# Optimization experiments

Measured on AMD Instinct MI355X. Metric: run time of the kernel, lower is better.

The kernel has to match this reference:

```python
import jax, jax.numpy as jnp
import numpy as np

N = 65536
D_MODEL = 8
D_STATE = 16
D_INNER = 16  # d_model * expand
PK = 12       # sqrt(144)
NE = 144
EH = 16
GH = 4
NH = 4
PEER_IN = GH + 2 * D_MODEL + 2   # 22
GRU_IN = 2 + 2 * D_MODEL          # 18
RESCALE = 0.1


def setup_inputs() -> dict:
    key = jax.random.key(0)
    ks = iter(jax.random.split(key, 40))
    rn = lambda shape, s=0.02: jax.random.normal(next(ks), shape, dtype=jnp.float32) * s
    inp = {
        'grad': jax.random.normal(next(ks), (N,), dtype=jnp.float32),
        'sharpness': jax.random.uniform(next(ks), (N,), dtype=jnp.float32),
        'gru_state': jnp.zeros((N, GH), jnp.float32),
        'mfwd_state': jnp.zeros((D_INNER, D_STATE), jnp.float32),
        'mbwd_state': jnp.zeros((D_INNER, D_STATE), jnp.float32),
        # input_proj: Linear(2, d_model, bias=True)
        'inproj_W': rn((D_MODEL, 2), 0.5), 'inproj_b': jnp.zeros((D_MODEL,), jnp.float32),
        # two Mamba3ScanBlocks stacked on leading axis: [0]=fwd, [1]=bwd
        'm_inW': rn((2, 2 * D_INNER, D_MODEL), 0.2),
        'm_dtW': rn((2, D_INNER, D_INNER), 0.2), 'm_dtb': jnp.zeros((2, D_INNER), jnp.float32),
        'm_BW': rn((2, D_STATE, D_INNER), 0.2), 'm_CW': rn((2, D_STATE, D_INNER), 0.2),
        'm_Alog': jnp.broadcast_to(jnp.log(jnp.linspace(1.0, D_STATE, D_STATE, dtype=jnp.float32))[None, None, :], (2, D_INNER, D_STATE)).copy(),
        'm_D': jnp.ones((2, D_INNER), jnp.float32),
        'm_rope': rn((2, D_INNER, D_STATE), 0.01),
        'm_outW': rn((2, D_MODEL, D_INNER), 0.2),
        # MiniGRU: Linear(22, 4) x3
        'gru_Wz': rn((GH, GRU_IN + GH), 0.2), 'gru_bz': jnp.zeros((GH,), jnp.float32),
        'gru_Wr': rn((GH, GRU_IN + GH), 0.2), 'gru_br': jnp.zeros((GH,), jnp.float32),
        'gru_Wh': rn((GH, GRU_IN + GH), 0.2), 'gru_bh': jnp.zeros((GH,), jnp.float32),
        # PEER heads (stacked over heads)
        'peer_qW': rn((NH, D_MODEL, PEER_IN), 0.2),
        'keysA': rn((NH, PK, D_MODEL // 2), 0.02),
        'keysB': rn((NH, PK, D_MODEL // 2), 0.02),
        # shared expert pool
        'eW1': rn((NE, EH, 1), 0.02), 'eb1': jnp.zeros((NE, EH), jnp.float32),
        'eW2': rn((NE, 1, EH), 0.02), 'eb2': jnp.zeros((NE, 1), jnp.float32),
    }
    return inp


def _mamba_scan(x, h0, inW, dtW, dtb, BW, CW, Alog, Dp, rope, outW):
    # x: [N, d_model]; h0: [d_inner, d_state]
    xz = x @ inW.T                       # [N, 2*d_inner]
    xb, z = xz[:, :D_INNER], xz[:, D_INNER:]
    dt = jax.nn.softplus(xb @ dtW.T + dtb)   # [N, d_inner]
    B = xb @ BW.T                            # [N, d_state]
    C = xb @ CW.T                            # [N, d_state]
    A = -jnp.exp(Alog)                       # [d_inner, d_state]

    def step(h, t):
        dt_i, B_i, C_i, xb_i = t
        dti = dt_i[:, None]                                # [d_inner, 1]
        A_bar = (1.0 + dti * A * 0.5) / (1.0 - dti * A * 0.5 + 1e-8)
        ph = dti * rope
        h_rot = h * jnp.cos(ph) - jnp.roll(h, 1, axis=-1) * jnp.sin(ph)
        h_new = A_bar * h_rot + (dti * B_i[None, :]) * xb_i[:, None]
        y = (h_new * C_i[None, :]).sum(-1)                 # [d_inner]
        return h_new, y

    h_final, ys = jax.lax.scan(step, h0, (dt, B, C, xb))
    y = ys * jax.nn.silu(z) + Dp[None, :] * xb
    return y @ outW.T, h_final


def reference(grad, sharpness, gru_state, mfwd_state, mbwd_state,
              inproj_W, inproj_b,
              m_inW, m_dtW, m_dtb, m_BW, m_CW, m_Alog, m_D, m_rope, m_outW,
              gru_Wz, gru_bz, gru_Wr, gru_br, gru_Wh, gru_bh,
              peer_qW, keysA, keysB, eW1, eb1, eW2, eb2):
    g = grad.reshape(-1).astype(jnp.float32)
    s = sharpness.reshape(-1).astype(jnp.float32)
    sort_idx = jnp.argsort(jnp.abs(g))
    gs, ss = g[sort_idx], s[sort_idx]

    x = jnp.stack([gs, ss], axis=-1) @ inproj_W.T + inproj_b   # [N, d_model]

    fwd_out, new_fwd = _mamba_scan(x, mfwd_state, m_inW[0], m_dtW[0], m_dtb[0],
                                   m_BW[0], m_CW[0], m_Alog[0], m_D[0], m_rope[0], m_outW[0])
    bwd_out, new_bwd = _mamba_scan(x[::-1], mbwd_state, m_inW[1], m_dtW[1], m_dtb[1],
                                   m_BW[1], m_CW[1], m_Alog[1], m_D[1], m_rope[1], m_outW[1])
    bwd_out = bwd_out[::-1]

    unsort = jnp.argsort(sort_idx)
    fwd_ctx = fwd_out[unsort]
    bwd_ctx = bwd_out[unsort]

    # MiniGRU
    gru_in = jnp.concatenate([g[:, None], s[:, None], fwd_ctx, bwd_ctx], axis=-1)  # [N, 18]
    h = gru_state.astype(jnp.float32)
    xh = jnp.concatenate([gru_in, h], axis=-1)
    zg = jax.nn.sigmoid(xh @ gru_Wz.T + gru_bz)
    r = jax.nn.sigmoid(xh @ gru_Wr.T + gru_br)
    xrh = jnp.concatenate([gru_in, r * h], axis=-1)
    h_t = jnp.tanh(xrh @ gru_Wh.T + gru_bh)
    new_gru = (1.0 - zg) * h + zg * h_t

    # PEER routing (4 heads, product keys)
    peer_in = jnp.concatenate([new_gru, fwd_ctx, bwd_ctx, g[:, None], s[:, None]], axis=-1)  # [N, 22]
    half = D_MODEL // 2
    total = jnp.zeros((g.shape[0], 1), jnp.float32)
    for hidx in range(NH):
        q = peer_in @ peer_qW[hidx].T                              # [N, d_model]
        idx_a = jnp.argmax(q[:, :half] @ keysA[hidx].T, axis=-1)   # [N]
        idx_b = jnp.argmax(q[:, half:] @ keysB[hidx].T, axis=-1)
        eidx = idx_a * PK + idx_b                                  # [N]
        z1 = jax.nn.relu(eW1[eidx][:, :, 0] * g[:, None] + eb1[eidx])   # [N, EH]
        out = (eW2[eidx][:, 0, :] * z1).sum(-1, keepdims=True) + eb2[eidx]
        total = total + out
    total = total / NH

    smart_grad = g + RESCALE * total[:, 0]
    return smart_grad.reshape(grad.shape), new_gru, new_fwd, new_bwd
```

## Files before the change

### kernel.cpp

```cpp
#include <hip/hip_runtime.h>
#include <math.h>

#define NTOT 65536
#define LCH 128
#define WRM 32
#define TILE 32
#define CCH 512
#define NBK 256
#define CAP2 512

typedef float f32x2 __attribute__((ext_vector_type(2)));
typedef float f32x4 __attribute__((ext_vector_type(4)));

__device__ __forceinline__ f32x2 mk2(float a, float b){ f32x2 r; r.x = a; r.y = b; return r; }
__device__ __forceinline__ f32x4 mk4(float a, float b, float c, float d){
  f32x4 r; r.x = a; r.y = b; r.z = c; r.w = d; return r; }
__device__ __forceinline__ f32x2 vlo(f32x4 v){ return __builtin_shufflevector(v, v, 0, 1); }
__device__ __forceinline__ f32x2 vhi(f32x4 v){ return __builtin_shufflevector(v, v, 2, 3); }

__device__ __forceinline__ f32x2 pk_fma(f32x2 a, f32x2 b, f32x2 c){
  return __builtin_elementwise_fma(a, b, c);
}
__device__ __forceinline__ f32x2 pk_fma_n0(f32x2 a, f32x2 b, f32x2 c){
  return __builtin_elementwise_fma(-a, b, c);
}
__device__ __forceinline__ f32x2 pk_mul(f32x2 a, f32x2 b){
  return a * b;
}

__device__ __forceinline__ float d_softplus(float x){
  return fmaxf(x, 0.f) + __logf(1.f + __expf(-fabsf(x)));
}
__device__ __forceinline__ float d_sigmoid(float x){
  return 1.f / (1.f + __expf(-x));
}
__device__ __forceinline__ float fast_rcp(float x){
  return __builtin_amdgcn_rcpf(x);
}
__device__ __forceinline__ float cheap_tanh(float x){
  float e = __expf(2.f*x);
  return fmaf(-2.f, fast_rcp(e + 1.f), 1.f);
}
template<int CTRL>
__device__ __forceinline__ float dpp_mov(float x){
  return __int_as_float(__builtin_amdgcn_update_dpp(0, __float_as_int(x), CTRL, 0xF, 0xF, true));
}

__device__ __forceinline__ float erfinv_f(float x){
  float w = -__logf((1.0f - x) * (1.0f + x));
  float p;
  if (w < 5.0f){
    w = w - 2.5f;
    p = 2.81022636e-08f;
    p = fmaf(p, w, 3.43273939e-07f);
    p = fmaf(p, w, -3.5233877e-06f);
    p = fmaf(p, w, -4.39150654e-06f);
    p = fmaf(p, w, 0.00021858087f);
    p = fmaf(p, w, -0.00125372503f);
    p = fmaf(p, w, -0.00417768164f);
    p = fmaf(p, w, 0.246640727f);
    p = fmaf(p, w, 1.50140941f);
  } else {
    w = sqrtf(w) - 3.0f;
    p = -0.000200214257f;
    p = fmaf(p, w, 0.000100950558f);
    p = fmaf(p, w, 0.00134934322f);
    p = fmaf(p, w, -0.00367342844f);
    p = fmaf(p, w, 0.00573950773f);
    p = fmaf(p, w, -0.0076224613f);
    p = fmaf(p, w, 0.00943887047f);
    p = fmaf(p, w, 1.00167406f);
    p = fmaf(p, w, 2.83297682f);
  }
  return p * x;
}

__global__ __launch_bounds__(512) void k_bucketsort(
    const float* __restrict__ g, unsigned* __restrict__ sidx)
{
  __shared__ unsigned long long buf[CAP2];
  __shared__ unsigned sred[512];
  __shared__ unsigned scnt;
  int t = threadIdx.x, blk = blockIdx.x;
  int lane = t & 63;
  unsigned kLo, kHi;
  if (blk == 0) kLo = 0u;
  else          kLo = __float_as_uint(1.41421356f * erfinv_f((float)blk * (1.0f/256.0f)));
  if (blk == NBK-1) kHi = 0x80000000u;
  else              kHi = __float_as_uint(1.41421356f * erfinv_f((float)(blk+1) * (1.0f/256.0f)));
  if (t == 0) scnt = 0u;
  __syncthreads();
  unsigned below_loc = 0;
  const float4* g4 = (const float4*)g;
  for (int r = 0; r < 32; ++r){
    int rr = (r + (blk & 31)) & 31;
    int i4 = rr*512 + t;
    float4 v = g4[i4];
    unsigned kk[4];
    kk[0] = __float_as_uint(v.x) & 0x7fffffffu;
    kk[1] = __float_as_uint(v.y) & 0x7fffffffu;
    kk[2] = __float_as_uint(v.z) & 0x7fffffffu;
    kk[3] = __float_as_uint(v.w) & 0x7fffffffu;
    unsigned idx0 = (unsigned)i4 * 4u;
    #pragma unroll
    for (int q = 0; q < 4; ++q){
      unsigned key = kk[q];
      below_loc += (key < kLo) ? 1u : 0u;
      bool in = (key >= kLo) && (key < kHi);
      unsigned long long mask = __ballot(in);
      if (in){
        unsigned prefix = (unsigned)__popcll(mask & ((1ull << lane) - 1ull));
        unsigned basep = 0u;
        if (prefix == 0u) basep = atomicAdd(&scnt, (unsigned)__popcll(mask));
        int leader = __ffsll((long long)mask) - 1;
        basep = __shfl(basep, leader, 64);
        unsigned p = basep + prefix;
        if (p < CAP2) buf[p] = ((unsigned long long)key << 16) | (idx0 + (unsigned)q);
      }
    }
  }
  sred[t] = below_loc;
  __syncthreads();
  unsigned cnt = scnt;
  if (cnt > CAP2) cnt = CAP2;
  for (int off = 256; off > 0; off >>= 1){
    if (t < off) sred[t] += sred[t + off];
    __syncthreads();
  }
  unsigned base = sred[0];
  if ((unsigned)t < cnt){
    unsigned long long val = buf[t];
    unsigned pos = 0u;
    for (unsigned m = 0; m < cnt; ++m)
      pos += (buf[m] < val) ? 1u : 0u;
    sidx[base + pos] = (unsigned)(val & 0xFFFFull);
  }
}

struct ScanK { f32x2 Ah2, nAh2, rp2, one2, cN2, cH2, c62, mone2; };

template<bool FWD, bool REAL, int I0>
__device__ __forceinline__ void scan_pairs(float& h,
    const f32x4* __restrict__ pkB, const f32x4* __restrict__ sbB,
    float* __restrict__ lvT, const f32x2* __restrict__ szdT,
    const ScanK& K, int s)
{
  float yv[4];
  #pragma unroll
  for (int i = I0; i < 16; ++i){
    const int mm = FWD ? i : 15 - i;
    f32x4 pk4 = pkB[mm];
    f32x4 sb4 = sbB[mm];
    f32x2 dt2 = vlo(pk4), dxb2 = vhi(pk4);
    f32x2 B2  = vlo(sb4), C2   = vhi(sb4);
    f32x2 num2 = pk_fma(dt2, K.Ah2,  K.one2);
    f32x2 den2 = pk_fma(dt2, K.nAh2, K.one2);
    f32x2 ph2  = pk_mul(dt2, K.rp2);
    f32x2 p22  = pk_mul(ph2, ph2);
    f32x2 w2   = pk_fma(p22, K.cN2, K.cH2);
    f32x2 cc2  = pk_fma_n0(p22, w2, K.one2);
    f32x2 si2  = pk_fma(p22, K.c62, K.mone2);
    f32x2 ns2  = pk_mul(ph2, si2);
    f32x2 db2  = pk_mul(dxb2, B2);
    float r0 = fast_rcp(den2.x), r1 = fast_rcp(den2.y);
    f32x2 Ab2 = mk2(num2.x * r0, num2.y * r1);
    f32x2 acv = pk_mul(Ab2, cc2);
    f32x2 asv = pk_mul(Ab2, ns2);
    const float ac_1 = FWD ? acv.x : acv.y, ac_2 = FWD ? acv.y : acv.x;
    const float as_1 = FWD ? asv.x : asv.y, as_2 = FWD ? asv.y : asv.x;
    const float d_1  = FWD ? db2.x : db2.y, d_2  = FWD ? db2.y : db2.x;
    const float C_1  = FWD ? C2.x  : C2.y,  C_2  = FWD ? C2.y  : C2.x;
    float hm = dpp_mov<0x121>(h);
    h = fmaf(ac_1, h, fmaf(as_1, hm, d_1));
    if (REAL){
      float v = h * C_1;
      v += dpp_mov<0xB1>(v);
      v += dpp_mov<0x4E>(v);
      v += dpp_mov<0x140>(v);
      v += dpp_mov<0x141>(v);
      yv[(2*i) & 3] = v;
    }
    hm = dpp_mov<0x121>(h);
    h = fmaf(ac_2, h, fmaf(as_2, hm, d_2));
    if (REAL){
      float v = h * C_2;
      v += dpp_mov<0xB1>(v);
      v += dpp_mov<0x4E>(v);
      v += dpp_mov<0x140>(v);
      v += dpp_mov<0x141>(v);
      yv[(2*i+1) & 3] = v;
      if ((i & 1) == 1 && s < 4){
        const int ms = 2*i + 1;
        const int row = FWD ? (ms - 3) : (34 - ms);
        float val = (s==0) ? yv[0] : ((s==1) ? yv[1] : ((s==2) ? yv[2] : yv[3]));
        f32x2 sd = szdT[row*18];
        lvT[row*20] = fmaf(val, sd.x, sd.y);
      }
    }
  }
}

__global__ __launch_bounds__(512, 4) void k_mega(
    const float* __restrict__ g, const float* __restrict__ sh,
    const unsigned* __restrict__ sidx,
    const float* __restrict__ inprojW, const float* __restrict__ inprojb,
    const float* __restrict__ m_inW, const float* __restrict__ m_dtW,
    const float* __restrict__ m_dtb, const float* __restrict__ m_BW,
    const float* __restrict__ m_CW,
    const float* __restrict__ Alog, const float* __restrict__ rope,
    const float* __restrict__ m_D, const float* __restrict__ m_outW,
    const float* __restrict__ mfwd, const float* __restrict__ mbwd,
    const float* __restrict__ gru_state,
    const float* __restrict__ Wz, const float* __restrict__ bz,
    const float* __restrict__ Wr, const float* __restrict__ br,
    const float* __restrict__ Wh, const float* __restrict__ bh,
    const float* __restrict__ qW, const float* __restrict__ kA, const float* __restrict__ kB,
    const float* __restrict__ eW1, const float* __restrict__ eb1,
    const float* __restrict__ eW2, const float* __restrict__ eb2,
    float* __restrict__ dout)
{
  __shared__ float wip[16], wipb[8];
  __shared__ float cXB[2*16*12], cDT[2*16*12], cB[2*16*12], cC[2*16*12], cZ[2*16*12];
  __shared__ float wdtb2[32], sD2[32], wOW2[256];
  __shared__ float gsAll[(LCH + 2*WRM)*2];
  __shared__ f32x4 PK2[2*16*17];
  __shared__ f32x4 SB2[2*16*17];
  __shared__ f32x2 SZD[2*TILE*18];
  __shared__ float ldsV[2*TILE*20];
  __shared__ float ctxT[2*LCH*12];
  __shared__ float sWz[88], sWr[88], sWh[88], sbz[4], sbr[4], sbh[4];
  __shared__ float sqW[704], skA[192], skB[192];
  __shared__ float hsum[LCH*4];

  int c = blockIdx.x;
  int t = threadIdx.x;
  int dir = t >> 8;
  int tt = t & 255;
  int d = tt >> 4, s = tt & 15;
  int e2 = tt >> 4, kq = tt & 15;

  if (t < 16) wip[t] = inprojW[t];
  if (t < 8)  wipb[t] = inprojb[t];
  if (t < 32){ wdtb2[t] = m_dtb[t]; sD2[t] = m_D[t]; }
  if (t < 256) wOW2[t] = m_outW[t];
  if (t < 256){
    int dd2 = t >> 7, rem = t & 127, k = rem >> 3, m = rem & 7;
    cXB[dd2*192 + k*12 + m] = m_inW[dd2*256 + k*8 + m];
    cZ [dd2*192 + k*12 + m] = m_inW[dd2*256 + (16+k)*8 + m];
  }
  for (int idx = t; idx < 768; idx += 512){
    int mat = idx >> 8, rem = idx & 255;
    int dd2 = rem >> 7, k = (rem >> 3) & 15, m = rem & 7;
    const float* wm = (mat==0) ? m_dtW : ((mat==1) ? m_BW : m_CW);
    float a = 0.f;
    #pragma unroll
    for (int j2 = 0; j2 < 16; ++j2)
      a = fmaf(wm[dd2*256 + k*16 + j2], m_inW[dd2*256 + j2*8 + m], a);
    float* dst = (mat==0) ? cDT : ((mat==1) ? cB : cC);
    dst[dd2*192 + k*12 + m] = a;
  }
  for (int k = t; k < 88; k += 512){ sWz[k]=Wz[k]; sWr[k]=Wr[k]; sWh[k]=Wh[k]; }
  if (t < 4){ sbz[t]=bz[t]; sbr[t]=br[t]; sbh[t]=bh[t]; }
  for (int k = t; k < 704; k += 512) sqW[k]=qW[k];
  for (int k = t; k < 192; k += 512){ skA[k]=kA[k]; skB[k]=kB[k]; }

  int base = c*LCH - WRM;
  for (int k = t; k < LCH + 2*WRM; k += 512){
    int p = base + k;
    p = p < 0 ? 0 : (p >= NTOT ? NTOT-1 : p);
    unsigned u = sidx[p];
    gsAll[k*2]   = g[u];
    gsAll[k*2+1] = sh[u];
  }

  float Ah = -__expf(Alog[dir*256 + tt]) * 0.5f;
  float rp = rope[dir*256 + tt];
  bool fwd = (dir == 0);
  bool bnd = (fwd && c == 0) || (!fwd && c == CCH-1);
  float h = 0.f;
  ScanK K;
  K.Ah2 = mk2(Ah, Ah); K.nAh2 = mk2(-Ah, -Ah); K.rp2 = mk2(rp, rp);
  K.one2 = mk2(1.f, 1.f); K.cN2 = mk2(-0.041666668f, -0.041666668f);
  K.cH2 = mk2(0.5f, 0.5f); K.c62 = mk2(0.16666667f, 0.16666667f);
  K.mone2 = mk2(-1.f, -1.f);
  const f32x4* pkB = &PK2[(dir*16 + d)*17];
  const f32x4* sbB = &SB2[(dir*16 + s)*17];
  float* lvF = &ldsV[dir*TILE*20 + d + s*20];
  float* lvB = &ldsV[dir*TILE*20 + d - s*20];
  const f32x2* szdF = (const f32x2*)SZD + dir*TILE*18 + d + s*18;
  const f32x2* szdB = (const f32x2*)SZD + dir*TILE*18 + d - s*18;
  __syncthreads();

  f32x2 rXB[4], rDT[4], rZ[4], rB[4], rC[4];
  #pragma unroll
  for (int p = 0; p < 4; ++p){
    int wb = dir*192 + kq*12 + 2*p;
    rXB[p] = *(const f32x2*)&cXB[wb];
    rDT[p] = *(const f32x2*)&cDT[wb];
    rZ [p] = *(const f32x2*)&cZ [wb];
    rB [p] = *(const f32x2*)&cB [wb];
    rC [p] = *(const f32x2*)&cC [wb];
  }
  f32x2 wgA[4], wgB[4], wb2[4];
  #pragma unroll
  for (int p = 0; p < 4; ++p){
    wgA[p] = mk2(wip[4*p],   wip[4*p+2]);
    wgB[p] = mk2(wip[4*p+1], wip[4*p+3]);
    wb2[p] = mk2(wipb[2*p],  wipb[2*p+1]);
  }
  float dtbk = wdtb2[dir*16 + kq];
  float Dk   = sD2[dir*16 + kq];

  auto do_proj = [&](int loff){
    int m0 = loff + 2*e2;
    f32x4 gs4 = *(const f32x4*)&gsAll[m0*2];
    f32x2 ge2 = mk2(gs4.x, gs4.x), se2 = mk2(gs4.y, gs4.y);
    f32x2 go2 = mk2(gs4.z, gs4.z), so2 = mk2(gs4.w, gs4.w);
    f32x2 xe[4], xo[4];
    #pragma unroll
    for (int p = 0; p < 4; ++p){
      xe[p] = pk_fma(wgA[p], ge2, pk_fma(wgB[p], se2, wb2[p]));
      xo[p] = pk_fma(wgA[p], go2, pk_fma(wgB[p], so2, wb2[p]));
    }
    f32x2 axb_e = mk2(0.f,0.f), axb_o = axb_e, adt_e = axb_e, adt_o = axb_e;
    f32x2 azz_e = axb_e, azz_o = axb_e, abb_e = axb_e, abb_o = axb_e;
    f32x2 acc_e = axb_e, acc_o = axb_e;
    #pragma unroll
    for (int p = 0; p < 4; ++p){
      axb_e = pk_fma(rXB[p], xe[p], axb_e);  axb_o = pk_fma(rXB[p], xo[p], axb_o);
      adt_e = pk_fma(rDT[p], xe[p], adt_e);  adt_o = pk_fma(rDT[p], xo[p], adt_o);
      azz_e = pk_fma(rZ [p], xe[p], azz_e);  azz_o = pk_fma(rZ [p], xo[p], azz_o);
      abb_e = pk_fma(rB [p], xe[p], abb_e);  abb_o = pk_fma(rB [p], xo[p], abb_o);
      acc_e = pk_fma(rC [p], xe[p], acc_e);  acc_o = pk_fma(rC [p], xo[p], acc_o);
    }
    float xb_e = axb_e.x + axb_e.y, xb_o = axb_o.x + axb_o.y;
    float dt_e = d_softplus(adt_e.x + adt_e.y + dtbk);
    float dt_o = d_softplus(adt_o.x + adt_o.y + dtbk);
    float zz_e = azz_e.x + azz_e.y, zz_o = azz_o.x + azz_o.y;
    float bb_e = abb_e.x + abb_e.y, bb_o = abb_o.x + abb_o.y;
    float cv_e = acc_e.x + acc_e.y, cv_o = acc_o.x + acc_o.y;
    int ridx = (dir*16 + kq)*17 + e2;
    PK2[ridx] = mk4(dt_e, dt_o, dt_e*xb_e, dt_o*xb_o);
    SB2[ridx] = mk4(bb_e, bb_o, cv_e, cv_o);
    SZD[(dir*TILE + 2*e2)*18 + kq]   = mk2(zz_e * d_sigmoid(zz_e), Dk*xb_e);
    SZD[(dir*TILE + 2*e2+1)*18 + kq] = mk2(zz_o * d_sigmoid(zz_o), Dk*xb_o);
  };

  auto do_outproj = [&](int lo){
    int pos = tt >> 3, mm8 = tt & 7;
    const f32x4* lv4 = (const f32x4*)&ldsV[(dir*TILE + pos)*20];
    const f32x4* ow4 = (const f32x4*)&wOW2[dir*128 + mm8*16];
    f32x2 acc2 = mk2(0.f, 0.f);
    #pragma unroll
    for (int q = 0; q < 4; ++q){
      f32x4 v4 = lv4[q], w4 = ow4[q];
      acc2 = pk_fma(vlo(w4), vlo(v4), acc2);
      acc2 = pk_fma(vhi(w4), vhi(v4), acc2);
    }
    ctxT[(dir*LCH + (lo - c*LCH + pos))*12 + mm8] = acc2.x + acc2.y;
  };

  {
    int loff = fwd ? 0 : (LCH + 2*WRM) - TILE;
    do_proj(loff);
    __syncthreads();
    if (fwd) scan_pairs<true,  false, 8>(h, pkB, sbB, lvF, szdF, K, s);
    else     scan_pairs<false, false, 8>(h, pkB, sbB, lvB, szdB, K, s);
    __syncthreads();
    if (bnd) h = fwd ? mfwd[tt] : mbwd[tt];
  }
  int prev_lo = 0;
  for (int j = 1; j < 5; ++j){
    int lo = fwd ? (base + j*TILE) : (base + (LCH + 2*WRM) - (j+1)*TILE);
    if (j > 1) do_outproj(prev_lo);
    do_proj(lo - base);
    __syncthreads();
    if (fwd) scan_pairs<true,  true, 0>(h, pkB, sbB, lvF, szdF, K, s);
    else     scan_pairs<false, true, 0>(h, pkB, sbB, lvB, szdB, K, s);
    __syncthreads();
    prev_lo = lo;
  }
  do_outproj(prev_lo);
  if (fwd && c == CCH-1)  dout[5*NTOT + tt] = h;
  if (!fwd && c == 0)     dout[5*NTOT + 256 + tt] = h;
  __syncthreads();

  {
    int elem = t >> 2, sub = t & 3;
    unsigned u = sidx[c*LCH + elem];
    float gi = gsAll[(WRM + elem)*2], si = gsAll[(WRM + elem)*2 + 1];
    f32x2 xin2[9];
    xin2[0] = mk2(gi, si);
    #pragma unroll
    for (int p = 0; p < 4; ++p){
      xin2[1+p] = *(const f32x2*)&ctxT[elem*12 + 2*p];
      xin2[5+p] = *(const f32x2*)&ctxT[(LCH + elem)*12 + 2*p];
    }
    f32x4 hv = *(const f32x4*)&gru_state[u*4u];
    int wb = sub*22;
    f32x2 az2 = mk2(0.f,0.f), ar2 = az2, ah2 = az2;
    #pragma unroll
    for (int i = 0; i < 9; ++i){
      az2 = pk_fma(*(const f32x2*)&sWz[wb+2*i], xin2[i], az2);
      ar2 = pk_fma(*(const f32x2*)&sWr[wb+2*i], xin2[i], ar2);
      ah2 = pk_fma(*(const f32x2*)&sWh[wb+2*i], xin2[i], ah2);
    }
    az2 = pk_fma(*(const f32x2*)&sWz[wb+18], vlo(hv), az2);
    az2 = pk_fma(*(const f32x2*)&sWz[wb+20], vhi(hv), az2);
    ar2 = pk_fma(*(const f32x2*)&sWr[wb+18], vlo(hv), ar2);
    ar2 = pk_fma(*(const f32x2*)&sWr[wb+20], vhi(hv), ar2);
    float zg = d_sigmoid(az2.x + az2.y + sbz[sub]);
    float rg = d_sigmoid(ar2.x + ar2.y + sbr[sub]);
    float h01 = (sub & 1) ? hv.y : hv.x;
    float h23 = (sub & 1) ? hv.w : hv.z;
    float hown = (sub & 2) ? h23 : h01;
    float rh = rg * hown;
    f32x2 rh01 = mk2(dpp_mov<0x00>(rh), dpp_mov<0x55>(rh));
    f32x2 rh23 = mk2(dpp_mov<0xAA>(rh), dpp_mov<0xFF>(rh));
    ah2 = pk_fma(*(const f32x2*)&sWh[wb+18], rh01, ah2);
    ah2 = pk_fma(*(const f32x2*)&sWh[wb+20], rh23, ah2);
    float ht = cheap_tanh(ah2.x + ah2.y + sbh[sub]);
    float ngo = fmaf(zg, ht - hown, hown);
    dout[NTOT + u*4u + (unsigned)sub] = ngo;
    f32x2 n01 = mk2(dpp_mov<0x00>(ngo), dpp_mov<0x55>(ngo));
    f32x2 n23 = mk2(dpp_mov<0xAA>(ngo), dpp_mov<0xFF>(ngo));
    float qv[8];
    #pragma unroll
    for (int o = 0; o < 8; ++o){
      int qb = sub*176 + o*22;
      f32x2 a2 = pk_fma(*(const f32x2*)&sqW[qb],   n01, mk2(0.f,0.f));
      a2 = pk_fma(*(const f32x2*)&sqW[qb+2], n23, a2);
      #pragma unroll
      for (int i = 0; i < 8; ++i)
        a2 = pk_fma(*(const f32x2*)&sqW[qb+4+2*i], xin2[1+i], a2);
      a2 = pk_fma(*(const f32x2*)&sqW[qb+20], xin2[0], a2);
      qv[o] = a2.x + a2.y;
    }
    int ia = 0; float best = -1e30f;
    #pragma unroll
    for (int k = 0; k < 12; ++k){
      int kb = sub*48 + k*4;
      float sc = skA[kb]*qv[0] + skA[kb+1]*qv[1] + skA[kb+2]*qv[2] + skA[kb+3]*qv[3];
      if (sc > best){ best = sc; ia = k; }
    }
    int ib = 0; best = -1e30f;
    #pragma unroll
    for (int k = 0; k < 12; ++k){
      int kb = sub*48 + k*4;
      float sc = skB[kb]*qv[4] + skB[kb+1]*qv[5] + skB[kb+2]*qv[6] + skB[kb+3]*qv[7];
      if (sc > best){ best = sc; ib = k; }
    }
    int e = ia*12 + ib;
    float outv = eb2[e];
    const float4* w14 = (const float4*)&eW1[e*16];
    const float4* b14 = (const float4*)&eb1[e*16];
    const float4* w24 = (const float4*)&eW2[e*16];
    #pragma unroll
    for (int q4 = 0; q4 < 4; ++q4){
      float4 a1 = w14[q4], a2 = b14[q4], a3 = w24[q4];
      float z1;
      z1 = fmaxf(fmaf(a1.x, gi, a2.x), 0.f); outv = fmaf(a3.x, z1, outv);
      z1 = fmaxf(fmaf(a1.y, gi, a2.y), 0.f); outv = fmaf(a3.y, z1, outv);
      z1 = fmaxf(fmaf(a1.z, gi, a2.z), 0.f); outv = fmaf(a3.z, z1, outv);
      z1 = fmaxf(fmaf(a1.w, gi, a2.w), 0.f); outv = fmaf(a3.w, z1, outv);
    }
    hsum[elem*4 + sub] = outv;
  }
  __syncthreads();
  if (t < LCH){
    float total = (hsum[t*4] + hsum[t*4+1] + hsum[t*4+2] + hsum[t*4+3])*0.25f;
    unsigned u = sidx[c*LCH + t];
    float gi = gsAll[(WRM + t)*2];
    dout[u] = gi + 0.1f*total;
  }
}

extern "C" void kernel_launch(void* const* d_in, const int* in_sizes, int n_in,
                              void* d_out, int out_size, void* d_ws, size_t ws_size,
                              hipStream_t stream)
{
  const float* grad     = (const float*)d_in[0];
  const float* sharp    = (const float*)d_in[1];
  const float* gru_st   = (const float*)d_in[2];
  const float* mfwd     = (const float*)d_in[3];
  const float* mbwd     = (const float*)d_in[4];
  const float* inprojW  = (const float*)d_in[5];
  const float* inprojb  = (const float*)d_in[6];
  const float* m_inW    = (const float*)d_in[7];
  const float* m_dtW    = (const float*)d_in[8];
  const float* m_dtb    = (const float*)d_in[9];
  const float* m_BW     = (const float*)d_in[10];
  const float* m_CW     = (const float*)d_in[11];
  const float* m_Alog   = (const float*)d_in[12];
  const float* m_D      = (const float*)d_in[13];
  const float* m_rope   = (const float*)d_in[14];
  const float* m_outW   = (const float*)d_in[15];
  const float* gWz      = (const float*)d_in[16];
  const float* gbz      = (const float*)d_in[17];
  const float* gWr      = (const float*)d_in[18];
  const float* gbr      = (const float*)d_in[19];
  const float* gWh      = (const float*)d_in[20];
  const float* gbh      = (const float*)d_in[21];
  const float* peer_qW  = (const float*)d_in[22];
  const float* keysA    = (const float*)d_in[23];
  const float* keysB    = (const float*)d_in[24];
  const float* eW1      = (const float*)d_in[25];
  const float* eb1      = (const float*)d_in[26];
  const float* eW2      = (const float*)d_in[27];
  const float* eb2      = (const float*)d_in[28];
  float* out = (float*)d_out;

  unsigned* sidx = (unsigned*)d_ws;

  k_bucketsort<<<NBK, 512, 0, stream>>>(grad, sidx);
  k_mega<<<CCH, 512, 0, stream>>>(grad, sharp, sidx,
      inprojW, inprojb, m_inW, m_dtW, m_dtb, m_BW, m_CW,
      m_Alog, m_rope, m_D, m_outW, mfwd, mbwd, gru_st,
      gWz, gbz, gWr, gbr, gWh, gbh, peer_qW, keysA, keysB,
      eW1, eb1, eW2, eb2, out);
}
```

Measured before the change: 176.6 us.

## Software-pipeline projection of next tile with current scan; simplify bucket-sort atomics

Splits the per-tile input projection into a compute step and an LDS write step. The next tile's projection is computed in registers while the current tile's scan runs, and an empty asm keeps those values live across the scan. This is meant to hide projection latency behind the serial scan, at the cost of higher register pressure. Separately, the bucket-sort kernel drops the wave-level ballot/prefix aggregation in favour of one LDS atomicAdd per element, and the rank-counting loop is unrolled.

```diff
diff --git a/kernel.cpp b/kernel.cpp
--- a/kernel.cpp
+++ b/kernel.cpp
@@ -82,7 +82,6 @@
   __shared__ unsigned sred[512];
   __shared__ unsigned scnt;
   int t = threadIdx.x, blk = blockIdx.x;
-  int lane = t & 63;
   unsigned kLo, kHi;
   if (blk == 0) kLo = 0u;
   else          kLo = __float_as_uint(1.41421356f * erfinv_f((float)blk * (1.0f/256.0f)));
@@ -106,15 +105,8 @@
     for (int q = 0; q < 4; ++q){
       unsigned key = kk[q];
       below_loc += (key < kLo) ? 1u : 0u;
-      bool in = (key >= kLo) && (key < kHi);
-      unsigned long long mask = __ballot(in);
-      if (in){
-        unsigned prefix = (unsigned)__popcll(mask & ((1ull << lane) - 1ull));
-        unsigned basep = 0u;
-        if (prefix == 0u) basep = atomicAdd(&scnt, (unsigned)__popcll(mask));
-        int leader = __ffsll((long long)mask) - 1;
-        basep = __shfl(basep, leader, 64);
-        unsigned p = basep + prefix;
+      if (key >= kLo && key < kHi){
+        unsigned p = atomicAdd(&scnt, 1u);
         if (p < CAP2) buf[p] = ((unsigned long long)key << 16) | (idx0 + (unsigned)q);
       }
     }
@@ -131,6 +123,7 @@
   if ((unsigned)t < cnt){
     unsigned long long val = buf[t];
     unsigned pos = 0u;
+    #pragma unroll 4
     for (unsigned m = 0; m < cnt; ++m)
       pos += (buf[m] < val) ? 1u : 0u;
     sidx[base + pos] = (unsigned)(val & 0xFFFFull);
@@ -138,6 +131,14 @@
 }
 
 struct ScanK { f32x2 Ah2, nAh2, rp2, one2, cN2, cH2, c62, mone2; };
+struct ProjR { float dt_e, dt_o, dxb_e, dxb_o, bb_e, bb_o, cv_e, cv_o,
+                     sz_e, sz_o, Db_e, Db_o; };
+
+__device__ __forceinline__ void keep_alive(const ProjR& r){
+  asm volatile("" :: "v"(r.dt_e), "v"(r.dt_o), "v"(r.dxb_e), "v"(r.dxb_o),
+                     "v"(r.bb_e), "v"(r.bb_o), "v"(r.cv_e), "v"(r.cv_o),
+                     "v"(r.sz_e), "v"(r.sz_o), "v"(r.Db_e), "v"(r.Db_o));
+}
 
 template<bool FWD, bool REAL, int I0>
 __device__ __forceinline__ void scan_pairs(float& h,
@@ -311,7 +312,7 @@
   float dtbk = wdtb2[dir*16 + kq];
   float Dk   = sD2[dir*16 + kq];
 
-  auto do_proj = [&](int loff){
+  auto proj_compute = [&](int loff)->ProjR{
     int m0 = loff + 2*e2;
     f32x4 gs4 = *(const f32x4*)&gsAll[m0*2];
     f32x2 ge2 = mk2(gs4.x, gs4.x), se2 = mk2(gs4.y, gs4.y);
@@ -334,16 +335,23 @@
       acc_e = pk_fma(rC [p], xe[p], acc_e);  acc_o = pk_fma(rC [p], xo[p], acc_o);
     }
     float xb_e = axb_e.x + axb_e.y, xb_o = axb_o.x + axb_o.y;
-    float dt_e = d_softplus(adt_e.x + adt_e.y + dtbk);
-    float dt_o = d_softplus(adt_o.x + adt_o.y + dtbk);
     float zz_e = azz_e.x + azz_e.y, zz_o = azz_o.x + azz_o.y;
-    float bb_e = abb_e.x + abb_e.y, bb_o = abb_o.x + abb_o.y;
-    float cv_e = acc_e.x + acc_e.y, cv_o = acc_o.x + acc_o.y;
+    ProjR r;
+    r.dt_e = d_softplus(adt_e.x + adt_e.y + dtbk);
+    r.dt_o = d_softplus(adt_o.x + adt_o.y + dtbk);
+    r.dxb_e = r.dt_e * xb_e;  r.dxb_o = r.dt_o * xb_o;
+    r.bb_e = abb_e.x + abb_e.y;  r.bb_o = abb_o.x + abb_o.y;
+    r.cv_e = acc_e.x + acc_e.y;  r.cv_o = acc_o.x + acc_o.y;
+    r.sz_e = zz_e * d_sigmoid(zz_e);  r.sz_o = zz_o * d_sigmoid(zz_o);
+    r.Db_e = Dk * xb_e;  r.Db_o = Dk * xb_o;
+    return r;
+  };
+  auto proj_write = [&](const ProjR& r){
     int ridx = (dir*16 + kq)*17 + e2;
-    PK2[ridx] = mk4(dt_e, dt_o, dt_e*xb_e, dt_o*xb_o);
-    SB2[ridx] = mk4(bb_e, bb_o, cv_e, cv_o);
-    SZD[(dir*TILE + 2*e2)*18 + kq]   = mk2(zz_e * d_sigmoid(zz_e), Dk*xb_e);
-    SZD[(dir*TILE + 2*e2+1)*18 + kq] = mk2(zz_o * d_sigmoid(zz_o), Dk*xb_o);
+    PK2[ridx] = mk4(r.dt_e, r.dt_o, r.dxb_e, r.dxb_o);
+    SB2[ridx] = mk4(r.bb_e, r.bb_o, r.cv_e, r.cv_o);
+    SZD[(dir*TILE + 2*e2)*18 + kq]   = mk2(r.sz_e, r.Db_e);
+    SZD[(dir*TILE + 2*e2+1)*18 + kq] = mk2(r.sz_o, r.Db_o);
   };
 
   auto do_outproj = [&](int lo){
@@ -361,22 +369,27 @@
   };
 
   {
-    int loff = fwd ? 0 : (LCH + 2*WRM) - TILE;
-    do_proj(loff);
-    __syncthreads();
-    if (fwd) scan_pairs<true,  false, 8>(h, pkB, sbB, lvF, szdF, K, s);
-    else     scan_pairs<false, false, 8>(h, pkB, sbB, lvB, szdB, K, s);
-    __syncthreads();
-    if (bnd) h = fwd ? mfwd[tt] : mbwd[tt];
-  }
+    ProjR P0 = proj_compute(fwd ? 0 : (LCH + 2*WRM) - TILE);
+    proj_write(P0);
+  }
+  __syncthreads();
+  ProjR P = proj_compute(fwd ? TILE : (LCH + 2*WRM) - 2*TILE);
+  if (fwd) scan_pairs<true,  false, 8>(h, pkB, sbB, lvF, szdF, K, s);
+  else     scan_pairs<false, false, 8>(h, pkB, sbB, lvB, szdB, K, s);
+  keep_alive(P);
+  __syncthreads();
+  if (bnd) h = fwd ? mfwd[tt] : mbwd[tt];
+
   int prev_lo = 0;
   for (int j = 1; j < 5; ++j){
     int lo = fwd ? (base + j*TILE) : (base + (LCH + 2*WRM) - (j+1)*TILE);
+    proj_write(P);
     if (j > 1) do_outproj(prev_lo);
-    do_proj(lo - base);
     __syncthreads();
+    if (j < 4) P = proj_compute(fwd ? (j+1)*TILE : (LCH + 2*WRM) - (j+2)*TILE);
     if (fwd) scan_pairs<true,  true, 0>(h, pkB, sbB, lvF, szdF, K, s);
     else     scan_pairs<false, true, 0>(h, pkB, sbB, lvB, szdB, K, s);
+    if (j < 4) keep_alive(P);
     __syncthreads();
     prev_lo = lo;
   }
```

Result: slower. 200.3 us (+13.4%).
